# Optimization experiments

Measured on AMD Instinct MI355X. Metric: run time of the kernel, lower is better.

## Reference

```python
import jax, jax.numpy as jnp
import numpy as np

B, L = 2048, 64
STOCH, DETER, OBS, HID, ACT = 30, 200, 200, 200, 6


def setup_inputs() -> dict:
    key = jax.random.key(0)
    ks = jax.random.split(key, 20)
    p = lambda k, shape: jax.random.normal(k, shape, dtype=jnp.float32) * 0.05
    return {
        'obs_feats': jax.random.normal(ks[0], (B, L, OBS), dtype=jnp.float32),
        'actions': jax.random.normal(ks[1], (B, L, ACT), dtype=jnp.float32),
        'noise': jax.random.normal(ks[2], (B, L, STOCH), dtype=jnp.float32),
        # GRUCell params (torch layout: weight [3*deter, in])
        'W_ih': p(ks[3], (3 * DETER, STOCH + ACT)),
        'b_ih': p(ks[4], (3 * DETER,)),
        'W_hh': p(ks[5], (3 * DETER, DETER)),
        'b_hh': p(ks[6], (3 * DETER,)),
        # prior_net: Linear(deter->hid), ReLU, Linear(hid->2*stoch)
        'pW1': p(ks[7], (HID, DETER)), 'pb1': p(ks[8], (HID,)),
        'pW2': p(ks[9], (2 * STOCH, HID)), 'pb2': p(ks[10], (2 * STOCH,)),
        # post_net: Linear(obs+deter->hid), ReLU, Linear(hid->2*stoch)
        'qW1': p(ks[11], (HID, OBS + DETER)), 'qb1': p(ks[12], (HID,)),
        'qW2': p(ks[13], (2 * STOCH, HID)), 'qb2': p(ks[14], (2 * STOCH,)),
        # to_next_s: Linear(stoch->stoch)
        'sW': p(ks[15], (STOCH, STOCH)), 'sb': p(ks[16], (STOCH,)),
    }


def _std(pre):
    return jnp.clip(jax.nn.softplus(pre) + 1e-5, 1e-4)


def reference(obs_feats, actions, noise,
              W_ih, b_ih, W_hh, b_hh,
              pW1, pb1, pW2, pb2,
              qW1, qb1, qW2, qb2,
              sW, sb):
    def step(carry, xs):
        h, s = carry
        obs, a, eps = xs  # [B,OBS], [B,ACT], [B,STOCH]
        x = jnp.concatenate([s, a], axis=-1)  # [B, STOCH+ACT]
        gi = x @ W_ih.T + b_ih
        gh = h @ W_hh.T + b_hh
        ir, iz, inn = jnp.split(gi, 3, axis=-1)
        hr, hz, hn = jnp.split(gh, 3, axis=-1)
        r = jax.nn.sigmoid(ir + hr)
        z = jax.nn.sigmoid(iz + hz)
        n = jnp.tanh(inn + r * hn)
        h_new = (1.0 - z) * n + z * h  # [B, DETER]
        # prior
        pp = jax.nn.relu(h_new @ pW1.T + pb1) @ pW2.T + pb2
        mu_p, pre_p = jnp.split(pp, 2, axis=-1)
        std_p = _std(pre_p)
        # posterior (concat obs_feat and h)
        qp = jax.nn.relu(jnp.concatenate([obs, h_new], axis=-1) @ qW1.T + qb1) @ qW2.T + qb2
        mu_q, pre_q = jnp.split(qp, 2, axis=-1)
        std_q = _std(pre_q)
        s_new = mu_q + std_q * eps  # reparameterize
        return (h_new, s_new), (mu_p, std_p, mu_q, std_q, s_new, h_new)

    h0 = jnp.zeros((obs_feats.shape[0], DETER), dtype=obs_feats.dtype)
    s0 = jnp.zeros((obs_feats.shape[0], STOCH), dtype=obs_feats.dtype)
    xs = (jnp.swapaxes(obs_feats, 0, 1),  # [L,B,OBS]
          jnp.swapaxes(actions, 0, 1),
          jnp.swapaxes(noise, 0, 1))
    _, ys = jax.lax.scan(step, (h0, s0), xs)
    # each y: [L, B, *] -> [B, L, *]; concat along feature dim -> [B, L, 4*STOCH+STOCH+DETER]
    out = jnp.concatenate([jnp.swapaxes(y, 0, 1) for y in ys], axis=-1)
    return out
```

## Files before the change

kernel.cpp:

```cpp
#include <hip/hip_runtime.h>


typedef unsigned short u16;
typedef unsigned int u32;
typedef __attribute__((ext_vector_type(8))) short short8;
typedef __attribute__((ext_vector_type(4))) float f32x4;

#define LL 64
#define OBS_ 200
#define ACT_ 6
#define STO 30
#define OUTC 350

#define U_WG   0
#define U_PW1  468
#define U_QW1  559
#define U_PW2  741
#define U_QW2  769
#define U_TOT  797
#define QX_OFF (1u << 20)

#define BAR() do { \
  asm volatile("s_waitcnt lgkmcnt(0)" ::: "memory"); \
  __builtin_amdgcn_s_barrier(); \
  __builtin_amdgcn_sched_barrier(0); \
} while (0)

__device__ __forceinline__ u16 f2b(float f){
  u32 u = __float_as_uint(f);
  u = (u + 0x7fffu + ((u >> 16) & 1u)) >> 16;
  return (u16)u;
}
__device__ __forceinline__ float b2f(u16 h){ return __uint_as_float(((u32)h) << 16); }

__device__ __forceinline__ short8 ldA7(const u16* buf, int r, int colStart){
  return *(const short8*)((const char*)buf + r*512 + ((colStart*2) ^ ((r & 7) << 4)));
}
__device__ __forceinline__ void st27(u16* buf, int r, int c, u16 v){
  *(u16*)((char*)buf + r*512 + ((c*2) ^ ((r & 7) << 4))) = v;
}
__device__ __forceinline__ u16 ld27(const u16* buf, int r, int c){
  return *(const u16*)((const char*)buf + r*512 + ((c*2) ^ ((r & 7) << 4)));
}
__device__ __forceinline__ short8 ldA3(const u16* buf, int r, int colStart){
  return *(const short8*)((const char*)buf + r*448 + ((colStart*2) ^ ((r & 3) << 4)));
}
__device__ __forceinline__ void st23(u16* buf, int r, int c, u16 v){
  *(u16*)((char*)buf + r*448 + ((c*2) ^ ((r & 3) << 4))) = v;
}
__device__ __forceinline__ void st8_3(u16* buf, int r, int c8, short8 v){
  *(short8*)((char*)buf + r*448 + ((c8*16) ^ ((r & 3) << 4))) = v;
}
__device__ __forceinline__ short8 ldB(const char* wsb, int unit, int lane){
  return *(const short8*)(wsb + (((size_t)unit) << 10) + ((size_t)lane << 4));
}
__device__ __forceinline__ short8 lwq(const u16* sw, int lu, int lane){
  return *(const short8*)((const char*)sw + ((size_t)lu << 10) + (lane << 4));
}
__device__ __forceinline__ f32x4 mfma(short8 a, short8 b, f32x4 c){
  return __builtin_amdgcn_mfma_f32_16x16x32_bf16(a, b, c, 0, 0, 0);
}
__device__ __forceinline__ float sigm(float x){ return 1.f / (1.f + __expf(-x)); }
__device__ __forceinline__ float tanhf_(float x){
  x = fminf(fmaxf(x, -15.f), 15.f);
  float e = __expf(-2.f * x);
  return (1.f - e) / (1.f + e);
}
__device__ __forceinline__ float softplus_(float x){
  return (x > 20.f) ? x : log1pf(__expf(x));
}
__device__ __forceinline__ short8 pack8(f32x4 a, f32x4 b){
  short8 v;
  v[0]=(short)f2b(a[0]); v[1]=(short)f2b(a[1]); v[2]=(short)f2b(a[2]); v[3]=(short)f2b(a[3]);
  v[4]=(short)f2b(b[0]); v[5]=(short)f2b(b[1]); v[6]=(short)f2b(b[2]); v[7]=(short)f2b(b[3]);
  return v;
}

__global__ __launch_bounds__(512) void pack_w(
    const float* W_ih, const float* W_hh, const float* pW1f, const float* qW1f,
    const float* pW2f, const float* qW2f, u16* wsu)
{
  int u = blockIdx.x;
  int t = threadIdx.x;
  int lane = t >> 3, j = t & 7;
  int nl = lane & 15, kg = lane >> 4;
  float v = 0.f;
  if (u < U_PW1) {
    int nt = u / 9, ks = u % 9;
    int k = ks*32 + kg*8 + j;
    int c = nt*16 + nl;
    int grow, part, coff;
    if (c < 208)      { grow = c;            part = 0; coff = c; }
    else if (c < 416) { grow = 200 + (c-208); part = 0; coff = c-208; }
    else if (c < 624) { grow = 400 + (c-416); part = 1; coff = c-416; }
    else              { grow = 400 + (c-624); part = 2; coff = c-624; }
    if (coff < 200) {
      if (k < 36)                  { if (part != 2) v = W_ih[grow*36 + k]; }
      else if (k >= 64 && k < 264) { if (part != 1) v = W_hh[grow*200 + (k-64)]; }
    }
  } else if (u < U_QW1) {
    int uu = u - U_PW1; int nt = uu / 7, ks = uu % 7;
    int k = ks*32 + kg*8 + j; int n = nt*16 + nl;
    if (n < 200 && k < 200) v = pW1f[n*200 + k];
  } else if (u < U_PW2) {
    int uu = u - U_QW1; int nt = uu / 14, ks = uu % 14;
    int k = ks*32 + kg*8 + j; int n = nt*16 + nl;
    if (n < 200) {
      if (k < 200) v = qW1f[n*400 + k];
      else if (k >= 224 && k < 424) v = qW1f[n*400 + 200 + (k-224)];
    }
  } else {
    bool isQ = (u >= U_QW2);
    int uu = u - (isQ ? U_QW2 : U_PW2); int nt = uu / 7, ks = uu % 7;
    int k = ks*32 + kg*8 + j; int c = nt*16 + nl;
    int row = (c < 32) ? c : 30 + (c - 32);
    bool ok = (c < 32) ? (c < 30) : ((c - 32) < 30);
    const float* W = isQ ? qW2f : pW2f;
    if (ok && k < 200) v = W[row*200 + k];
  }
  wsu[((size_t)u << 9) + lane*8 + j] = f2b(v);
}

__global__ __launch_bounds__(512) void qx_k(
    const float* __restrict__ obs, const float* __restrict__ qb1,
    const char* __restrict__ wsb, u16* __restrict__ qxp)
{
  const int tid = threadIdx.x, w = tid >> 6, lane = tid & 63;
  const int nl = lane & 15, kg = lane >> 4;
  const int r0 = blockIdx.x * 16;
  __shared__ __align__(16) u16 sob[16*224];
  for (int i = tid; i < 16*224; i += 512) sob[i] = 0;
  __syncthreads();
  if (tid < 400) {
    int m = tid / 25, c8 = tid % 25;
    const float* op = obs + (size_t)(r0+m)*OBS_ + c8*8;
    f32x4 a = *(const f32x4*)op, b = *(const f32x4*)(op + 4);
    st8_3(sob, m, c8, pack8(a, b));
  }
  __syncthreads();
#pragma unroll
  for (int qi = 0; qi < 2; ++qi) {
    int tq = w + qi*8;
    if (tq < 13) {
      f32x4 acc{0,0,0,0};
#pragma unroll
      for (int ks = 0; ks < 7; ++ks)
        acc = mfma(ldA3(sob, nl, ks*32 + kg*8), ldB(wsb, U_QW1 + tq*14 + ks, lane), acc);
      int n = tq*16 + nl;
      if (n < 200) {
        float b = qb1[n];
#pragma unroll
        for (int i = 0; i < 4; ++i)
          qxp[(size_t)(r0 + kg*4 + i)*OBS_ + n] = f2b(acc[i] + b);
      }
    }
  }
}

__global__ __launch_bounds__(512) void prior_k(
    const float* __restrict__ pb1, const float* __restrict__ pb2,
    const char* __restrict__ wsb, float* __restrict__ out)
{
  const int tid = threadIdx.x, w = tid >> 6, lane = tid & 63;
  const int nl = lane & 15, kg = lane >> 4;
  const int r0 = blockIdx.x * 16;
  __shared__ __align__(16) u16 shh[16*224];
  __shared__ __align__(16) u16 spp[16*224];
  for (int i = tid; i < 16*224; i += 512) { shh[i] = 0; spp[i] = 0; }
  __syncthreads();
  if (tid < 400) {
    int m = tid / 25, c8 = tid % 25;
    const float* hp = out + (size_t)(r0+m)*OUTC + 150 + c8*8;
    f32x4 a, b;
#pragma unroll
    for (int i = 0; i < 4; ++i) { a[i] = hp[i]; b[i] = hp[4+i]; }
    st8_3(shh, m, c8, pack8(a, b));
  }
  __syncthreads();
#pragma unroll
  for (int qi = 0; qi < 2; ++qi) {
    int tq = w + qi*8;
    if (tq < 13) {
      f32x4 acc{0,0,0,0};
#pragma unroll
      for (int ks = 0; ks < 7; ++ks)
        acc = mfma(ldA3(shh, nl, ks*32 + kg*8), ldB(wsb, U_PW1 + tq*7 + ks, lane), acc);
      int n = tq*16 + nl;
      if (n < 200) {
        float b = pb1[n];
#pragma unroll
        for (int i = 0; i < 4; ++i) {
          float v = acc[i] + b;
          st23(spp, kg*4 + i, n, f2b(v > 0.f ? v : 0.f));
        }
      }
    }
  }
  __syncthreads();
  if (w < 2) {
    f32x4 a0{0,0,0,0}, a1{0,0,0,0};
#pragma unroll
    for (int ks = 0; ks < 7; ++ks) {
      short8 af = ldA3(spp, nl, ks*32 + kg*8);
      a0 = mfma(af, ldB(wsb, U_PW2 + w*7 + ks,     lane), a0);
      a1 = mfma(af, ldB(wsb, U_PW2 + (w+2)*7 + ks, lane), a1);
    }
    int c3 = w*16 + nl;
    if (c3 < 30) {
      float bmu = pb2[c3], bpre = pb2[30 + c3];
#pragma unroll
      for (int i = 0; i < 4; ++i) {
        size_t ob = (size_t)(r0 + kg*4 + i)*OUTC;
        out[ob + c3] = a0[i] + bmu;
        float sp = softplus_(a1[i] + bpre) + 1e-5f;
        out[ob + 30 + c3] = fmaxf(sp, 1e-4f);
      }
    }
  }
}

__global__ __launch_bounds__(512, 2) void rssm_seq(
    const float* __restrict__ act, const float* __restrict__ noise,
    const float* __restrict__ b_ih, const float* __restrict__ b_hh,
    const float* __restrict__ qb2,
    const u16* __restrict__ qxp, const char* __restrict__ wsb,
    float* __restrict__ out)
{
  const int tid  = threadIdx.x;
  const int w    = tid >> 6;
  const int lane = tid & 63;
  const int nl   = lane & 15;
  const int kg   = lane >> 4;
  const int m0   = blockIdx.x * 16;

  __shared__ __align__(16) u16 swq[119*512];
  __shared__ __align__(16) u16 h0 [16*256];
  __shared__ __align__(16) u16 h1 [16*256];
  __shared__ __align__(16) u16 sqq[16*224];

  for (int i = tid; i < 16*256; i += 512) { h0[i]=0; h1[i]=0; }
  for (int i = tid; i < 16*224; i += 512) sqq[i]=0;
  for (int c = tid; c < 119*64; c += 512) {
    int lu = c >> 6, l16 = c & 63;
    int gu = (lu < 91) ? (U_QW1 + (lu/7)*14 + 7 + (lu%7)) : (U_QW2 + (lu - 91));
    *(short8*)((char*)swq + (size_t)c*16) =
        *(const short8*)(wsb + ((size_t)gu << 10) + (l16 << 4));
  }

  const int  cj  = w*16 + nl;
  const bool j2  = (w >= 3);
  const int  tq2 = w + 5;
  const int  cj2 = tq2*16 + nl;
  const bool cj2v = j2 && (cj2 < 200);
  const float bR1 = b_ih[cj]       + b_hh[cj];
  const float bZ1 = b_ih[200 + cj] + b_hh[200 + cj];
  const float bI1 = b_ih[400 + cj];
  const float bH1 = b_hh[400 + cj];
  float bR2=0,bZ2=0,bI2=0,bH2=0;
  if (cj2v) {
    bR2 = b_ih[cj2] + b_hh[cj2];
    bZ2 = b_ih[200+cj2] + b_hh[200+cj2];
    bI2 = b_ih[400+cj2];
    bH2 = b_hh[400+cj2];
  }
  const bool isP3 = (w < 2);
  const int  c3   = w*16 + nl;
  const bool c3v  = isP3 && (c3 < 30);
  float b3mu=0, b3pre=0;
  if (c3v) { b3mu = qb2[c3]; b3pre = qb2[30 + c3]; }
  const int  t2 = (w - 2)*64 + lane;
  const bool isAct = (w == 2 || w == 3) && (t2 < 96);

  __syncthreads();
  if (tid < 96) {
    int m = tid / 6, j = tid % 6;
    st27(h0, m, 230 + j, f2b(act[(size_t)(m0+m)*LL*ACT_ + j]));
  }
  __syncthreads();

#pragma unroll 1
  for (int l = 0; l < LL; ++l) {
    u16* hO = (l & 1) ? h1 : h0;
    u16* hN = (l & 1) ? h0 : h1;

    float ep[4] = {0,0,0,0};
    if (c3v && l > 0) {
      const float* np = noise + (size_t)(m0 + kg*4)*LL*STO + (size_t)(l-1)*STO + c3;
#pragma unroll
      for (int i = 0; i < 4; ++i) ep[i] = np[(size_t)i*LL*STO];
    }
    float qx1[4], qx2[4] = {0,0,0,0};
#pragma unroll
    for (int i = 0; i < 4; ++i)
      qx1[i] = b2f(qxp[((size_t)(m0 + kg*4 + i)*LL + l)*OBS_ + cj]);
    if (cj2v) {
#pragma unroll
      for (int i = 0; i < 4; ++i)
        qx2[i] = b2f(qxp[((size_t)(m0 + kg*4 + i)*LL + l)*OBS_ + cj2]);
    }
    float av = 0.f;
    if (isAct && (l + 1 < LL))
      av = act[((size_t)(m0 + t2/6)*LL + (l+1))*ACT_ + (t2 % 6)];

    short8 a7[7];
#pragma unroll
    for (int j = 0; j < 7; ++j) a7[j] = ldA7(hO, nl, j*32 + kg*8);

    f32x4 hr1{0,0,0,0}, hz1{0,0,0,0}, hn1{0,0,0,0};
    f32x4 hr2{0,0,0,0}, hz2{0,0,0,0}, hn2{0,0,0,0};
#pragma unroll
    for (int j = 0; j < 7; ++j) {
      hr1 = mfma(a7[j], ldB(wsb, U_WG + w*9 + 2 + j,      lane), hr1);
      hz1 = mfma(a7[j], ldB(wsb, U_WG + (13+w)*9 + 2 + j, lane), hz1);
      hn1 = mfma(a7[j], ldB(wsb, U_WG + (39+w)*9 + 2 + j, lane), hn1);
      if (j2) {
        hr2 = mfma(a7[j], ldB(wsb, U_WG + tq2*9 + 2 + j,      lane), hr2);
        hz2 = mfma(a7[j], ldB(wsb, U_WG + (13+tq2)*9 + 2 + j, lane), hz2);
        hn2 = mfma(a7[j], ldB(wsb, U_WG + (39+tq2)*9 + 2 + j, lane), hn2);
      }
    }
    if (isP3 && l > 0) {
      f32x4 q0{0,0,0,0}, q1a{0,0,0,0};
#pragma unroll
      for (int ks = 0; ks < 7; ++ks) {
        short8 af = ldA3(sqq, nl, ks*32 + kg*8);
        q0  = mfma(af, lwq(swq, 91 + w*7 + ks,     lane), q0);
        q1a = mfma(af, lwq(swq, 91 + (w+2)*7 + ks, lane), q1a);
      }
      if (c3 < 30) {
#pragma unroll
        for (int i = 0; i < 4; ++i) {
          int m = kg*4 + i;
          size_t ob = (size_t)(m0+m)*LL*OUTC + (size_t)(l-1)*OUTC;
          float mu = q0[i] + b3mu;
          float sp = softplus_(q1a[i] + b3pre) + 1e-5f;
          float sd = fmaxf(sp, 1e-4f);
          float s = mu + sd*ep[i];
          out[ob +  60 + c3] = mu;
          out[ob +  90 + c3] = sd;
          out[ob + 120 + c3] = s;
          st27(hO, m, 200 + c3, f2b(s));
        }
      }
    }
    BAR();

    {
      short8 x0 = ldA7(hO, nl, 200 + kg*8);
      short8 x1 = ldA7(hO, nl, 232 + kg*8);
      f32x4 aI1{0,0,0,0}, aI2{0,0,0,0};
      hr1 = mfma(x0, ldB(wsb, U_WG + w*9 + 0,      lane), hr1);
      hr1 = mfma(x1, ldB(wsb, U_WG + w*9 + 1,      lane), hr1);
      hz1 = mfma(x0, ldB(wsb, U_WG + (13+w)*9 + 0, lane), hz1);
      hz1 = mfma(x1, ldB(wsb, U_WG + (13+w)*9 + 1, lane), hz1);
      aI1 = mfma(x0, ldB(wsb, U_WG + (26+w)*9 + 0, lane), aI1);
      aI1 = mfma(x1, ldB(wsb, U_WG + (26+w)*9 + 1, lane), aI1);
      if (j2) {
        hr2 = mfma(x0, ldB(wsb, U_WG + tq2*9 + 0,      lane), hr2);
        hr2 = mfma(x1, ldB(wsb, U_WG + tq2*9 + 1,      lane), hr2);
        hz2 = mfma(x0, ldB(wsb, U_WG + (13+tq2)*9 + 0, lane), hz2);
        hz2 = mfma(x1, ldB(wsb, U_WG + (13+tq2)*9 + 1, lane), hz2);
        aI2 = mfma(x0, ldB(wsb, U_WG + (26+tq2)*9 + 0, lane), aI2);
        aI2 = mfma(x1, ldB(wsb, U_WG + (26+tq2)*9 + 1, lane), aI2);
      }
#pragma unroll
      for (int i = 0; i < 4; ++i) {
        int m = kg*4 + i;
        float r = sigm(hr1[i] + bR1);
        float z = sigm(hz1[i] + bZ1);
        float n = tanhf_(aI1[i] + bI1 + r*(hn1[i] + bH1));
        float hold = b2f(ld27(hO, m, cj));
        float hnew = (1.f - z)*n + z*hold;
        st27(hN, m, cj, f2b(hnew));
        out[(size_t)(m0+m)*LL*OUTC + (size_t)l*OUTC + 150 + cj] = hnew;
      }
      if (cj2v) {
#pragma unroll
        for (int i = 0; i < 4; ++i) {
          int m = kg*4 + i;
          float r = sigm(hr2[i] + bR2);
          float z = sigm(hz2[i] + bZ2);
          float n = tanhf_(aI2[i] + bI2 + r*(hn2[i] + bH2));
          float hold = b2f(ld27(hO, m, cj2));
          float hnew = (1.f - z)*n + z*hold;
          st27(hN, m, cj2, f2b(hnew));
          out[(size_t)(m0+m)*LL*OUTC + (size_t)l*OUTC + 150 + cj2] = hnew;
        }
      }
    }
    BAR();

    {
      short8 g[7];
#pragma unroll
      for (int ks = 0; ks < 7; ++ks) g[ks] = ldA7(hN, nl, ks*32 + kg*8);
      f32x4 aq1{0,0,0,0}, aq2{0,0,0,0};
#pragma unroll
      for (int ks = 0; ks < 7; ++ks) {
        aq1 = mfma(g[ks], lwq(swq, w*7 + ks, lane), aq1);
        if (j2) aq2 = mfma(g[ks], lwq(swq, tq2*7 + ks, lane), aq2);
      }
#pragma unroll
      for (int i = 0; i < 4; ++i) {
        int m = kg*4 + i;
        float v = aq1[i] + qx1[i];
        st23(sqq, m, cj, f2b(v > 0.f ? v : 0.f));
      }
      if (cj2v) {
#pragma unroll
        for (int i = 0; i < 4; ++i) {
          int m = kg*4 + i;
          float v = aq2[i] + qx2[i];
          st23(sqq, m, cj2, f2b(v > 0.f ? v : 0.f));
        }
      }
      if (isAct && (l + 1 < LL))
        st27(hN, t2/6, 230 + (t2 % 6), f2b(av));
    }
    BAR();
  }

  if (isP3) {
    float ep[4] = {0,0,0,0};
    if (c3v) {
      const float* np = noise + (size_t)(m0 + kg*4)*LL*STO + (size_t)(LL-1)*STO + c3;
#pragma unroll
      for (int i = 0; i < 4; ++i) ep[i] = np[(size_t)i*LL*STO];
    }
    f32x4 q0{0,0,0,0}, q1a{0,0,0,0};
#pragma unroll
    for (int ks = 0; ks < 7; ++ks) {
      short8 af = ldA3(sqq, nl, ks*32 + kg*8);
      q0  = mfma(af, lwq(swq, 91 + w*7 + ks,     lane), q0);
      q1a = mfma(af, lwq(swq, 91 + (w+2)*7 + ks, lane), q1a);
    }
    if (c3 < 30) {
#pragma unroll
      for (int i = 0; i < 4; ++i) {
        int m = kg*4 + i;
        size_t ob = (size_t)(m0+m)*LL*OUTC + (size_t)(LL-1)*OUTC;
        float mu = q0[i] + b3mu;
        float sp = softplus_(q1a[i] + b3pre) + 1e-5f;
        float sd = fmaxf(sp, 1e-4f);
        out[ob +  60 + c3] = mu;
        out[ob +  90 + c3] = sd;
        out[ob + 120 + c3] = mu + sd*ep[i];
      }
    }
  }
}

extern "C" void kernel_launch(void* const* d_in, const int* in_sizes, int n_in,
                              void* d_out, int out_size, void* d_ws, size_t ws_size,
                              hipStream_t stream) {
  const float* obs   = (const float*)d_in[0];
  const float* act   = (const float*)d_in[1];
  const float* noise = (const float*)d_in[2];
  const float* W_ih  = (const float*)d_in[3];
  const float* b_ih  = (const float*)d_in[4];
  const float* W_hh  = (const float*)d_in[5];
  const float* b_hh  = (const float*)d_in[6];
  const float* pW1   = (const float*)d_in[7];
  const float* pb1   = (const float*)d_in[8];
  const float* pW2   = (const float*)d_in[9];
  const float* pb2   = (const float*)d_in[10];
  const float* qW1   = (const float*)d_in[11];
  const float* qb1   = (const float*)d_in[12];
  const float* qW2   = (const float*)d_in[13];
  const float* qb2   = (const float*)d_in[14];
  float* out = (float*)d_out;
  u16* qxp = (u16*)((char*)d_ws + QX_OFF);

  pack_w<<<U_TOT, 512, 0, stream>>>(W_ih, W_hh, pW1, qW1, pW2, qW2, (u16*)d_ws);
  qx_k<<<8192, 512, 0, stream>>>(obs, qb1, (const char*)d_ws, qxp);
  rssm_seq<<<128, 512, 0, stream>>>(act, noise, b_ih, b_hh, qb2,
                                    qxp, (const char*)d_ws, out);
  prior_k<<<8192, 512, 0, stream>>>(pb1, pb2, (const char*)d_ws, out);
}
```

Before: 733.0 us.

## Spread GRU tiles over 12 waves and prefetch input-gate weights before barrier

The sequential RSSM kernel grows from 8 to 12 wavefronts per block, so each wave owns one GRU column tile (only wave 11 takes a second tile) instead of waves 3-7 each taking two. This shortens the per-step critical path inside the recurrent loop. The input-projection weight fragments are also loaded into registers before the mid-step barrier, which hides global-load latency behind the posterior computation. In exchange there are more waves per block and more live registers under a tighter launch bound. Any code that still assumes 8 waves or uses a 512 stride could mis-split work.

```diff
diff --git a/kernel.cpp b/kernel.cpp
--- a/kernel.cpp
+++ b/kernel.cpp
@@ -219,7 +219,7 @@
   }
 }
 
-__global__ __launch_bounds__(512, 2) void rssm_seq(
+__global__ __launch_bounds__(768, 3) void rssm_seq(
     const float* __restrict__ act, const float* __restrict__ noise,
     const float* __restrict__ b_ih, const float* __restrict__ b_hh,
     const float* __restrict__ qb2,
@@ -238,9 +238,9 @@
   __shared__ __align__(16) u16 h1 [16*256];
   __shared__ __align__(16) u16 sqq[16*224];
 
-  for (int i = tid; i < 16*256; i += 512) { h0[i]=0; h1[i]=0; }
-  for (int i = tid; i < 16*224; i += 512) sqq[i]=0;
-  for (int c = tid; c < 119*64; c += 512) {
+  for (int i = tid; i < 16*256; i += 768) { h0[i]=0; h1[i]=0; }
+  for (int i = tid; i < 16*224; i += 768) sqq[i]=0;
+  for (int c = tid; c < 119*64; c += 768) {
     int lu = c >> 6, l16 = c & 63;
     int gu = (lu < 91) ? (U_QW1 + (lu/7)*14 + 7 + (lu%7)) : (U_QW2 + (lu - 91));
     *(short8*)((char*)swq + (size_t)c*16) =
@@ -248,8 +248,8 @@
   }
 
   const int  cj  = w*16 + nl;
-  const bool j2  = (w >= 3);
-  const int  tq2 = w + 5;
+  const bool j2  = (w == 11);
+  const int  tq2 = 12;
   const int  cj2 = tq2*16 + nl;
   const bool cj2v = j2 && (cj2 < 200);
   const float bR1 = b_ih[cj]       + b_hh[cj];
@@ -319,6 +319,21 @@
         hn2 = mfma(a7[j], ldB(wsb, U_WG + (39+tq2)*9 + 2 + j, lane), hn2);
       }
     }
+    short8 xw1[6], xw2[6];
+    xw1[0] = ldB(wsb, U_WG + w*9 + 0,      lane);
+    xw1[1] = ldB(wsb, U_WG + w*9 + 1,      lane);
+    xw1[2] = ldB(wsb, U_WG + (13+w)*9 + 0, lane);
+    xw1[3] = ldB(wsb, U_WG + (13+w)*9 + 1, lane);
+    xw1[4] = ldB(wsb, U_WG + (26+w)*9 + 0, lane);
+    xw1[5] = ldB(wsb, U_WG + (26+w)*9 + 1, lane);
+    if (j2) {
+      xw2[0] = ldB(wsb, U_WG + tq2*9 + 0,      lane);
+      xw2[1] = ldB(wsb, U_WG + tq2*9 + 1,      lane);
+      xw2[2] = ldB(wsb, U_WG + (13+tq2)*9 + 0, lane);
+      xw2[3] = ldB(wsb, U_WG + (13+tq2)*9 + 1, lane);
+      xw2[4] = ldB(wsb, U_WG + (26+tq2)*9 + 0, lane);
+      xw2[5] = ldB(wsb, U_WG + (26+tq2)*9 + 1, lane);
+    }
     if (isP3 && l > 0) {
       f32x4 q0{0,0,0,0}, q1a{0,0,0,0};
 #pragma unroll
@@ -349,19 +364,13 @@
       short8 x0 = ldA7(hO, nl, 200 + kg*8);
       short8 x1 = ldA7(hO, nl, 232 + kg*8);
       f32x4 aI1{0,0,0,0}, aI2{0,0,0,0};
-      hr1 = mfma(x0, ldB(wsb, U_WG + w*9 + 0,      lane), hr1);
-      hr1 = mfma(x1, ldB(wsb, U_WG + w*9 + 1,      lane), hr1);
-      hz1 = mfma(x0, ldB(wsb, U_WG + (13+w)*9 + 0, lane), hz1);
-      hz1 = mfma(x1, ldB(wsb, U_WG + (13+w)*9 + 1, lane), hz1);
-      aI1 = mfma(x0, ldB(wsb, U_WG + (26+w)*9 + 0, lane), aI1);
-      aI1 = mfma(x1, ldB(wsb, U_WG + (26+w)*9 + 1, lane), aI1);
+      hr1 = mfma(x0, xw1[0], hr1);  hr1 = mfma(x1, xw1[1], hr1);
+      hz1 = mfma(x0, xw1[2], hz1);  hz1 = mfma(x1, xw1[3], hz1);
+      aI1 = mfma(x0, xw1[4], aI1);  aI1 = mfma(x1, xw1[5], aI1);
       if (j2) {
-        hr2 = mfma(x0, ldB(wsb, U_WG + tq2*9 + 0,      lane), hr2);
-        hr2 = mfma(x1, ldB(wsb, U_WG + tq2*9 + 1,      lane), hr2);
-        hz2 = mfma(x0, ldB(wsb, U_WG + (13+tq2)*9 + 0, lane), hz2);
-        hz2 = mfma(x1, ldB(wsb, U_WG + (13+tq2)*9 + 1, lane), hz2);
-        aI2 = mfma(x0, ldB(wsb, U_WG + (26+tq2)*9 + 0, lane), aI2);
-        aI2 = mfma(x1, ldB(wsb, U_WG + (26+tq2)*9 + 1, lane), aI2);
+        hr2 = mfma(x0, xw2[0], hr2);  hr2 = mfma(x1, xw2[1], hr2);
+        hz2 = mfma(x0, xw2[2], hz2);  hz2 = mfma(x1, xw2[3], hz2);
+        aI2 = mfma(x0, xw2[4], aI2);  aI2 = mfma(x1, xw2[5], aI2);
       }
 #pragma unroll
       for (int i = 0; i < 4; ++i) {
@@ -473,7 +482,7 @@
 
   pack_w<<<U_TOT, 512, 0, stream>>>(W_ih, W_hh, pW1, qW1, pW2, qW2, (u16*)d_ws);
   qx_k<<<8192, 512, 0, stream>>>(obs, qb1, (const char*)d_ws, qxp);
-  rssm_seq<<<128, 512, 0, stream>>>(act, noise, b_ih, b_hh, qb2,
+  rssm_seq<<<128, 768, 0, stream>>>(act, noise, b_ih, b_hh, qb2,
                                     qxp, (const char*)d_ws, out);
   prior_k<<<8192, 512, 0, stream>>>(pb1, pb2, (const char*)d_ws, out);
 }
```

Result: slower. 1.526 ms (+108.3%).
